# Kernel tuning notes

Hardware: AMD Instinct MI355X
Metric: run time of the kernel (lower is better)

The kernel has to match this reference:

```python
import math
import jax, jax.numpy as jnp
import numpy as np

N_HEAD = 16

def setup_inputs() -> dict:
    key = jax.random.key(0)
    k1, k2, k3 = jax.random.split(key, 3)
    B, T, C = 4, 2048, 1024
    x = jax.random.normal(k1, (B, T, C), dtype=jnp.float32)
    Wqkv = jax.random.normal(k2, (C, 3 * C), dtype=jnp.float32) * (1.0 / math.sqrt(C))
    bqkv = jnp.zeros((3 * C,), dtype=jnp.float32)
    Wproj = jax.random.normal(k3, (C, C), dtype=jnp.float32) * (1.0 / math.sqrt(C))
    bproj = jnp.zeros((C,), dtype=jnp.float32)
    return {"x": x, "Wqkv": Wqkv, "bqkv": bqkv, "Wproj": Wproj, "bproj": bproj}

def reference(x, Wqkv, bqkv, Wproj, bproj):
    B, T, C = x.shape
    H = N_HEAD
    D = C // H
    # fused QKV projection
    qkv = x @ Wqkv + bqkv                      # [B,T,3C]
    qkv = qkv.reshape(B, T, 3, H, D).transpose(0, 2, 3, 1, 4)  # [B,3,H,T,D]
    q, k, v = qkv[:, 0], qkv[:, 1], qkv[:, 2]  # each [B,H,T,D]
    scale = 1.0 / math.sqrt(D)
    att = jnp.einsum('bhtd,bhsd->bhts', q, k) * scale  # [B,H,T,T]
    # causal mask: disallow s > t
    mask = jnp.triu(jnp.ones((T, T), dtype=bool), k=1)
    att = jnp.where(mask, jnp.float32(-1e9), att)
    att = jax.nn.softmax(att, axis=-1)
    y = jnp.einsum('bhts,bhsd->bhtd', att, v)  # [B,H,T,D]
    y = y.transpose(0, 2, 1, 3).reshape(B, T, C)
    y = y @ Wproj + bproj
    return y
```

## Files before the change

### kernel.cpp

```cpp
#include <hip/hip_runtime.h>
#include <hip/hip_bf16.h>

#define B_ 4
#define T_ 2048
#define C_ 1024
#define H_ 16
#define D_ 64

typedef __attribute__((ext_vector_type(8))) short short8;
typedef __attribute__((ext_vector_type(4))) float f32x4;

#define QSCALE 0.18033688011112042f

static __device__ __forceinline__ unsigned short f2bf(float f) {
  unsigned u = __float_as_uint(f);
  u += 0x7fff + ((u >> 16) & 1);
  return (unsigned short)(u >> 16);
}

static __device__ __forceinline__ unsigned cvt_pk_bf16(float lo, float hi) {
  unsigned r;
  asm("v_cvt_pk_bf16_f32 %0, %1, %2" : "=v"(r) : "v"(lo), "v"(hi));
  return r;
}

static __device__ __forceinline__ float fast_exp2(float x) {
#if __has_builtin(__builtin_amdgcn_exp2f)
  return __builtin_amdgcn_exp2f(x);
#else
  return exp2f(x);
#endif
}

#define GL2LDS16(g, l)                                              \
  __builtin_amdgcn_global_load_lds(                                 \
      (const __attribute__((address_space(1))) void*)(g),           \
      (__attribute__((address_space(3))) void*)(l), 16, 0, 0)

__global__ __launch_bounds__(256) void prepass(
    const float* __restrict__ x, const float* __restrict__ Wq,
    const float* __restrict__ Wp, ushort* __restrict__ xb,
    ushort* __restrict__ Wqt, ushort* __restrict__ Wpt) {
  __shared__ ushort tile[32][33];
  const int bid = blockIdx.x;
  if (bid < 8192) {
    const size_t i = ((size_t)bid * 256 + threadIdx.x) * 4;
    float4 vv = *(const float4*)(x + i);
    ushort4 o = {f2bf(vv.x), f2bf(vv.y), f2bf(vv.z), f2bf(vv.w)};
    *(ushort4*)(xb + i) = o;
    return;
  }
  const float* in;
  ushort* out;
  int N, tix;
  if (bid < 8192 + 3072) {
    in = Wq; out = Wqt; N = 3 * C_; tix = bid - 8192;
  } else {
    in = Wp; out = Wpt; N = C_; tix = bid - 11264;
  }
  const int nT = N >> 5;
  const int k0 = (tix / nT) << 5, n0 = (tix % nT) << 5;
  const int r = threadIdx.x >> 3;
  const int c4 = (threadIdx.x & 7) << 2;
  float4 v = *(const float4*)(in + (size_t)(k0 + r) * N + n0 + c4);
  tile[c4 + 0][r] = f2bf(v.x);
  tile[c4 + 1][r] = f2bf(v.y);
  tile[c4 + 2][r] = f2bf(v.z);
  tile[c4 + 3][r] = f2bf(v.w);
  __syncthreads();
  ushort4 o = {tile[r][c4], tile[r][c4 + 1], tile[r][c4 + 2], tile[r][c4 + 3]};
  *(ushort4*)(out + (size_t)(n0 + r) * C_ + k0 + c4) = o;
}

static __device__ __forceinline__ void swz_src64(int wave, int lane, int p,
                                                 int& row, int& offU) {
  const int flat = p * 4096 + wave * 1024 + lane * 16;
  row = flat >> 7;
  const int pos = (flat & 127) >> 4;
  const int x = pos ^ (row & 7);
  offU = x * 8;
}
static __device__ __forceinline__ int swz_frag64(int r, int quad, int ko) {
  return r * 128 + (((quad | (ko << 2)) ^ (r & 7)) << 4);
}

__global__ __launch_bounds__(512, 2) void gemm_qkv_mfma(
    const ushort* __restrict__ A, const ushort* __restrict__ Bt,
    const float* __restrict__ bias, ushort* __restrict__ q,
    ushort* __restrict__ k, ushort* __restrict__ v) {
  __shared__ __align__(16) ushort KA[3][128 * 64];
  __shared__ __align__(16) ushort KB[3][256 * 64];
  const int wave = threadIdx.x >> 6, lane = threadIdx.x & 63;
  const int c = lane & 15, quad = lane >> 4;
  const int wm = wave >> 2, wn = wave & 3;
  const int bid0 = blockIdx.x;
  const int bid = (bid0 & 7) * 96 + (bid0 >> 3);
  const int m0 = (bid / 12) << 7;
  const int n0 = (bid % 12) << 8;

  int aRow[2], aX[2], bRow[4], bX[4];
#pragma unroll
  for (int p = 0; p < 2; ++p) {
    const int flat = p * 8192 + (int)threadIdx.x * 16;
    aRow[p] = flat >> 7;
    aX[p] = (((flat & 127) >> 4) ^ (aRow[p] & 7)) * 8;
  }
#pragma unroll
  for (int p = 0; p < 4; ++p) {
    const int flat = p * 8192 + (int)threadIdx.x * 16;
    bRow[p] = flat >> 7;
    bX[p] = (((flat & 127) >> 4) ^ (bRow[p] & 7)) * 8;
  }
  int fOffA[2][4], fOffB[2][4];
#pragma unroll
  for (int ko = 0; ko < 2; ++ko) {
#pragma unroll
    for (int i = 0; i < 4; ++i)
      fOffA[ko][i] = swz_frag64(wm * 64 + i * 16 + c, quad, ko);
#pragma unroll
    for (int j = 0; j < 4; ++j)
      fOffB[ko][j] = swz_frag64(wn * 64 + j * 16 + c, quad, ko);
  }

  f32x4 acc[4][4];
#pragma unroll
  for (int i = 0; i < 4; ++i)
#pragma unroll
    for (int j = 0; j < 4; ++j) acc[i][j] = (f32x4){0.f, 0.f, 0.f, 0.f};

#pragma unroll
  for (int p = 0; p < 4; ++p)
    GL2LDS16(Bt + (size_t)(n0 + bRow[p]) * C_ + bX[p],
             (char*)KB[0] + p * 8192 + wave * 1024);
#pragma unroll
  for (int p = 0; p < 2; ++p)
    GL2LDS16(A + (size_t)(m0 + aRow[p]) * C_ + aX[p],
             (char*)KA[0] + p * 8192 + wave * 1024);
#pragma unroll
  for (int p = 0; p < 4; ++p)
    GL2LDS16(Bt + (size_t)(n0 + bRow[p]) * C_ + 64 + bX[p],
             (char*)KB[1] + p * 8192 + wave * 1024);
#pragma unroll
  for (int p = 0; p < 2; ++p)
    GL2LDS16(A + (size_t)(m0 + aRow[p]) * C_ + 64 + aX[p],
             (char*)KA[1] + p * 8192 + wave * 1024);
  asm volatile("s_waitcnt vmcnt(6)" ::: "memory");
  __builtin_amdgcn_s_barrier();

  short8 af[4][2], bfA[2][2], bfB[2][2];
  {
    const char* la0 = (const char*)KA[0];
    const char* lb0 = (const char*)KB[0];
#pragma unroll
    for (int i = 0; i < 4; ++i)
#pragma unroll
      for (int ko = 0; ko < 2; ++ko)
        af[i][ko] = *(const short8*)(la0 + fOffA[ko][i]);
#pragma unroll
    for (int d = 0; d < 2; ++d)
#pragma unroll
      for (int ko = 0; ko < 2; ++ko)
        bfA[d][ko] = *(const short8*)(lb0 + fOffB[ko][d]);
  }

  int cur = 0;
  for (int kt = 0; kt < 16; ++kt) {
    const int nxt = (cur == 2) ? 0 : cur + 1;
    const int s2 = (nxt == 2) ? 0 : nxt + 1;
    const char* lb = (const char*)KB[cur];
    const int kk2 = (kt + 2) << 6;
    const bool more = (kt + 2) < 16;

#pragma unroll
    for (int d = 0; d < 2; ++d)
#pragma unroll
      for (int ko = 0; ko < 2; ++ko)
        bfB[d][ko] = *(const short8*)(lb + fOffB[ko][2 + d]);
    if (more) {
      GL2LDS16(Bt + (size_t)(n0 + bRow[0]) * C_ + kk2 + bX[0],
               (char*)KB[s2] + 0 * 8192 + wave * 1024);
      GL2LDS16(Bt + (size_t)(n0 + bRow[1]) * C_ + kk2 + bX[1],
               (char*)KB[s2] + 1 * 8192 + wave * 1024);
      GL2LDS16(A + (size_t)(m0 + aRow[0]) * C_ + kk2 + aX[0],
               (char*)KA[s2] + 0 * 8192 + wave * 1024);
    }
    __builtin_amdgcn_s_setprio(1);
#pragma unroll
    for (int i = 0; i < 4; ++i)
#pragma unroll
      for (int dj = 0; dj < 2; ++dj)
#pragma unroll
        for (int ko = 0; ko < 2; ++ko)
          acc[i][dj] = __builtin_amdgcn_mfma_f32_16x16x32_bf16(
              af[i][ko], bfA[dj][ko], acc[i][dj], 0, 0, 0);
    __builtin_amdgcn_s_setprio(0);

    if (more)
      asm volatile("s_waitcnt vmcnt(3) lgkmcnt(0)" ::: "memory");
    else
      asm volatile("s_waitcnt vmcnt(0) lgkmcnt(0)" ::: "memory");
    __builtin_amdgcn_s_barrier();

    short8 afN[4][2], bfAN[2][2];
    if (kt + 1 < 16) {
      const char* lan = (const char*)KA[nxt];
      const char* lbn = (const char*)KB[nxt];
#pragma unroll
      for (int i = 0; i < 4; ++i)
#pragma unroll
        for (int ko = 0; ko < 2; ++ko)
          afN[i][ko] = *(const short8*)(lan + fOffA[ko][i]);
#pragma unroll
      for (int d = 0; d < 2; ++d)
#pragma unroll
        for (int ko = 0; ko < 2; ++ko)
          bfAN[d][ko] = *(const short8*)(lbn + fOffB[ko][d]);
    }
    if (more) {
      GL2LDS16(Bt + (size_t)(n0 + bRow[2]) * C_ + kk2 + bX[2],
               (char*)KB[s2] + 2 * 8192 + wave * 1024);
      GL2LDS16(Bt + (size_t)(n0 + bRow[3]) * C_ + kk2 + bX[3],
               (char*)KB[s2] + 3 * 8192 + wave * 1024);
      GL2LDS16(A + (size_t)(m0 + aRow[1]) * C_ + kk2 + aX[1],
               (char*)KA[s2] + 1 * 8192 + wave * 1024);
    }
    __builtin_amdgcn_s_setprio(1);
#pragma unroll
    for (int i = 0; i < 4; ++i)
#pragma unroll
      for (int dj = 0; dj < 2; ++dj)
#pragma unroll
        for (int ko = 0; ko < 2; ++ko)
          acc[i][2 + dj] = __builtin_amdgcn_mfma_f32_16x16x32_bf16(
              af[i][ko], bfB[dj][ko], acc[i][2 + dj], 0, 0, 0);
    __builtin_amdgcn_s_setprio(0);
    if (kt + 1 < 16) {
#pragma unroll
      for (int i = 0; i < 4; ++i)
#pragma unroll
        for (int ko = 0; ko < 2; ++ko) af[i][ko] = afN[i][ko];
#pragma unroll
      for (int d = 0; d < 2; ++d)
#pragma unroll
        for (int ko = 0; ko < 2; ++ko) bfA[d][ko] = bfAN[d][ko];
    }
    cur = nxt;
  }

  const int s = n0 >> 10;
  if (s == 2) {
#pragma unroll
    for (int j = 0; j < 4; ++j) {
      const int n = n0 + wn * 64 + j * 16 + c;
      const int h = (n >> 6) & 15, d = n & 63;
      const float bval = bias[n];
#pragma unroll
      for (int i = 0; i < 4; ++i) {
        const int m = m0 + wm * 64 + i * 16 + quad * 4;
        const int b = m >> 11, t = m & 2047;
        ushort4 pk = {f2bf(acc[i][j][0] + bval), f2bf(acc[i][j][1] + bval),
                      f2bf(acc[i][j][2] + bval), f2bf(acc[i][j][3] + bval)};
        *(ushort4*)(v + (((size_t)((b << 4) + h) << 6) + d) * T_ + t) = pk;
      }
    }
  } else {
    ushort* outp = (s == 0) ? q : k;
    const float sc = (s == 0) ? QSCALE : 1.0f;
#pragma unroll
    for (int j = 0; j < 4; ++j) {
      const int n = n0 + wn * 64 + j * 16 + c;
      const int h = (n >> 6) & 15, d = n & 63;
      const float bval = bias[n];
#pragma unroll
      for (int i = 0; i < 4; ++i) {
#pragma unroll
        for (int r = 0; r < 4; ++r) {
          const int m = m0 + wm * 64 + i * 16 + quad * 4 + r;
          const int b = m >> 11, t = m & 2047;
          outp[(((size_t)((b << 4) + h) << 11) + t) * 64 + d] =
              f2bf((acc[i][j][r] + bval) * sc);
        }
      }
    }
  }
}

__global__ __launch_bounds__(256) void gemm_proj_mfma(
    const ushort* __restrict__ A, const ushort* __restrict__ Bt,
    const float* __restrict__ bias, float* __restrict__ out) {
  __shared__ __align__(16) ushort As[2][128 * 64];
  __shared__ __align__(16) ushort Bs[2][128 * 64];
  const int tid = threadIdx.x;
  const int wave = tid >> 6, lane = tid & 63;
  const int c = lane & 15, quad = lane >> 4;
  const int wm = wave & 1, wn = wave >> 1;
  const int bid0 = blockIdx.y * 8 + blockIdx.x;
  const int bid = (bid0 & 7) * 64 + (bid0 >> 3);
  const int m0 = (bid >> 3) << 7;
  const int n0 = (bid & 7) << 7;

  int sRow[4], sOff[4];
#pragma unroll
  for (int p = 0; p < 4; ++p) swz_src64(wave, lane, p, sRow[p], sOff[p]);
  int fOffA[2][4], fOffB[2][4];
#pragma unroll
  for (int ko = 0; ko < 2; ++ko) {
#pragma unroll
    for (int i = 0; i < 4; ++i)
      fOffA[ko][i] = swz_frag64(wm * 64 + i * 16 + c, quad, ko);
#pragma unroll
    for (int j = 0; j < 4; ++j)
      fOffB[ko][j] = swz_frag64(wn * 64 + j * 16 + c, quad, ko);
  }

  f32x4 acc[4][4];
#pragma unroll
  for (int i = 0; i < 4; ++i)
#pragma unroll
    for (int j = 0; j < 4; ++j) acc[i][j] = (f32x4){0.f, 0.f, 0.f, 0.f};

#define PROJ_STAGE(buf, kk)                                            \
  do {                                                                 \
    _Pragma("unroll") for (int p = 0; p < 4; ++p) {                    \
      GL2LDS16(A + (size_t)(m0 + sRow[p]) * C_ + (kk) + sOff[p],       \
               (char*)As[buf] + p * 4096 + wave * 1024);               \
      GL2LDS16(Bt + (size_t)(n0 + sRow[p]) * C_ + (kk) + sOff[p],      \
               (char*)Bs[buf] + p * 4096 + wave * 1024);               \
    }                                                                  \
  } while (0)

  PROJ_STAGE(0, 0);
  int cur = 0;
  for (int k0 = 0; k0 < C_; k0 += 64) {
    __syncthreads();
    if (k0 + 64 < C_) PROJ_STAGE(cur ^ 1, k0 + 64);
#pragma unroll
    for (int ko = 0; ko < 2; ++ko) {
      short8 af[4], bf[4];
#pragma unroll
      for (int i = 0; i < 4; ++i)
        af[i] = *(const short8*)((const char*)As[cur] + fOffA[ko][i]);
#pragma unroll
      for (int j = 0; j < 4; ++j)
        bf[j] = *(const short8*)((const char*)Bs[cur] + fOffB[ko][j]);
      __builtin_amdgcn_s_setprio(1);
#pragma unroll
      for (int i = 0; i < 4; ++i)
#pragma unroll
        for (int j = 0; j < 4; ++j)
          acc[i][j] = __builtin_amdgcn_mfma_f32_16x16x32_bf16(af[i], bf[j],
                                                              acc[i][j], 0, 0, 0);
      __builtin_amdgcn_s_setprio(0);
    }
    cur ^= 1;
  }
#undef PROJ_STAGE

#pragma unroll
  for (int j = 0; j < 4; ++j) {
    const int n = n0 + wn * 64 + j * 16 + c;
    const float bval = bias[n];
#pragma unroll
    for (int i = 0; i < 4; ++i) {
#pragma unroll
      for (int r = 0; r < 4; ++r) {
        const int m = m0 + wm * 64 + i * 16 + quad * 4 + r;
        out[(size_t)m * C_ + n] = acc[i][j][r] + bval;
      }
    }
  }
}

__global__ __launch_bounds__(256) void attn(const ushort* __restrict__ q,
                                            const ushort* __restrict__ k,
                                            const ushort* __restrict__ v,
                                            ushort* __restrict__ y2) {
  const int qt = 15 - (int)(blockIdx.x >> 6);
  const int bh = blockIdx.x & 63;
  const int t0 = qt << 7;
  const int w = threadIdx.x >> 6;
  const int lane = threadIdx.x & 63;
  const int c = lane & 15;
  const int quad = lane >> 4;

  const ushort* qp = q + (size_t)bh * T_ * D_;
  const ushort* kp = k + (size_t)bh * T_ * D_;
  const ushort* vp = v + (size_t)bh * D_ * T_;

  __shared__ __align__(16) ushort Ks[2][64 * 64];
  __shared__ __align__(16) ushort Vs[2][64 * 64];
  __shared__ __align__(16) ushort Ps[4][32][72];

  short8 qf[2][2];
#pragma unroll
  for (int g = 0; g < 2; ++g) {
    const ushort* qrow = qp + (size_t)(t0 + 32 * w + 16 * g + c) * D_;
    qf[g][0] = *(const short8*)(qrow + quad * 8);
    qf[g][1] = *(const short8*)(qrow + 32 + quad * 8);
  }

  int sRow[2], sX[2];
#pragma unroll
  for (int p = 0; p < 2; ++p) {
    const int flat = p * 4096 + (int)threadIdx.x * 16;
    sRow[p] = flat >> 7;
    sX[p] = (((flat & 127) >> 4) ^ (sRow[p] & 7)) * 8;
  }

#define STAGE(buf, s0s)                                                   \
  do {                                                                    \
    _Pragma("unroll") for (int p = 0; p < 2; ++p) {                       \
      GL2LDS16(kp + (size_t)((s0s) + sRow[p]) * D_ + sX[p],               \
               (char*)Ks[buf] + p * 4096 + w * 1024);                     \
      GL2LDS16(vp + (size_t)sRow[p] * T_ + (s0s) + sX[p],                 \
               (char*)Vs[buf] + p * 4096 + w * 1024);                     \
    }                                                                     \
  } while (0)

  f32x4 o[2][4];
  float l_i[2] = {0.f, 0.f};
#pragma unroll
  for (int g = 0; g < 2; ++g)
#pragma unroll
    for (int dt = 0; dt < 4; ++dt) o[g][dt] = (f32x4){0.f, 0.f, 0.f, 0.f};

  const int nb = 2 * qt + 2;
  STAGE(0, 0);
  int cur = 0;

  for (int ib = 0; ib < nb; ++ib) {
    const int s0 = ib << 6;
    __syncthreads();
    if (ib + 1 < nb) STAGE(cur ^ 1, s0 + 64);

    f32x4 st[2][4];
    __builtin_amdgcn_s_setprio(1);
#pragma unroll
    for (int kt = 0; kt < 4; ++kt) {
      const char* kb = (const char*)Ks[cur];
      short8 af0 = *(const short8*)(kb + swz_frag64(kt * 16 + c, quad, 0));
      short8 af1 = *(const short8*)(kb + swz_frag64(kt * 16 + c, quad, 1));
#pragma unroll
      for (int g = 0; g < 2; ++g) {
        f32x4 a = (f32x4){0.f, 0.f, 0.f, 0.f};
        a = __builtin_amdgcn_mfma_f32_16x16x32_bf16(af0, qf[g][0], a, 0, 0, 0);
        a = __builtin_amdgcn_mfma_f32_16x16x32_bf16(af1, qf[g][1], a, 0, 0, 0);
        st[g][kt] = a;
      }
    }
    __builtin_amdgcn_s_setprio(0);

#pragma unroll
    for (int g = 0; g < 2; ++g) {
      const int qbase = t0 + 32 * w + 16 * g;
      if (s0 + 63 > qbase) {
#pragma unroll
        for (int kt = 0; kt < 4; ++kt)
#pragma unroll
          for (int r = 0; r < 4; ++r)
            if (s0 + kt * 16 + 4 * quad + r > qbase + c) st[g][kt][r] = -1e30f;
      }
      float lacc = 0.f;
#pragma unroll
      for (int kt = 0; kt < 4; ++kt) {
        float p0 = fast_exp2(st[g][kt][0]);
        float p1 = fast_exp2(st[g][kt][1]);
        float p2 = fast_exp2(st[g][kt][2]);
        float p3 = fast_exp2(st[g][kt][3]);
        lacc += (p0 + p1) + (p2 + p3);
        uint2 pw = {cvt_pk_bf16(p0, p1), cvt_pk_bf16(p2, p3)};
        *(uint2*)(&Ps[w][g * 16 + c][kt * 16 + 4 * quad]) = pw;
      }
      l_i[g] += lacc;
    }

    short8 pf[2][2];
#pragma unroll
    for (int g = 0; g < 2; ++g) {
      pf[g][0] = *(const short8*)(&Ps[w][g * 16 + c][quad * 8]);
      pf[g][1] = *(const short8*)(&Ps[w][g * 16 + c][32 + quad * 8]);
    }
    __builtin_amdgcn_s_setprio(1);
#pragma unroll
    for (int dt = 0; dt < 4; ++dt) {
      const char* vb = (const char*)Vs[cur];
      short8 vf0 = *(const short8*)(vb + swz_frag64(dt * 16 + c, quad, 0));
      short8 vf1 = *(const short8*)(vb + swz_frag64(dt * 16 + c, quad, 1));
#pragma unroll
      for (int g = 0; g < 2; ++g) {
        o[g][dt] =
            __builtin_amdgcn_mfma_f32_16x16x32_bf16(vf0, pf[g][0], o[g][dt], 0, 0, 0);
        o[g][dt] =
            __builtin_amdgcn_mfma_f32_16x16x32_bf16(vf1, pf[g][1], o[g][dt], 0, 0, 0);
      }
    }
    __builtin_amdgcn_s_setprio(0);
    cur ^= 1;
  }
#undef STAGE

  float linv[2];
#pragma unroll
  for (int g = 0; g < 2; ++g) {
    float ls = l_i[g];
    ls += __shfl_xor(ls, 16);
    ls += __shfl_xor(ls, 32);
    linv[g] = 1.0f / ls;
  }

  const int b = bh >> 4, h = bh & 15;
#pragma unroll
  for (int g = 0; g < 2; ++g) {
    const int row = t0 + 32 * w + 16 * g + c;
    ushort* dst = y2 + (size_t)(b * T_ + row) * C_ + h * 64;
#pragma unroll
    for (int dt = 0; dt < 4; ++dt) {
      uint2 ov = {cvt_pk_bf16(o[g][dt][0] * linv[g], o[g][dt][1] * linv[g]),
                  cvt_pk_bf16(o[g][dt][2] * linv[g], o[g][dt][3] * linv[g])};
      *(uint2*)(dst + dt * 16 + 4 * quad) = ov;
    }
  }
}

extern "C" void kernel_launch(void* const* d_in, const int* in_sizes, int n_in,
                              void* d_out, int out_size, void* d_ws,
                              size_t ws_size, hipStream_t stream) {
  const float* x = (const float*)d_in[0];
  const float* Wqkv = (const float*)d_in[1];
  const float* bqkv = (const float*)d_in[2];
  const float* Wproj = (const float*)d_in[3];
  const float* bproj = (const float*)d_in[4];
  float* out = (float*)d_out;

  const size_t per = (size_t)B_ * H_ * T_ * D_;
  ushort* q = (ushort*)d_ws;
  ushort* k = q + per;
  ushort* v = k + per;
  ushort* y2 = v + per;
  ushort* xb = y2 + per;
  ushort* Wqkvt = xb + per;
  ushort* Wprojt = Wqkvt + 3 * C_ * C_;

  prepass<<<dim3(12288), 256, 0, stream>>>(x, Wqkv, Wproj, xb, Wqkvt, Wprojt);
  gemm_qkv_mfma<<<dim3(768), 512, 0, stream>>>(xb, Wqkvt, bqkv, q, k, v);
  attn<<<dim3(1024), 256, 0, stream>>>(q, k, v, y2);
  gemm_proj_mfma<<<dim3(8, 64), 256, 0, stream>>>(y2, Wprojt, bproj, out);
}
```

Measured before the change: 238.2 us.

## Use persistent attention blocks with atomic work queue and XCD-aware QKV tile mapping

```diff
diff --git a/kernel.cpp b/kernel.cpp
--- a/kernel.cpp
+++ b/kernel.cpp
@@ -40,9 +40,11 @@
 __global__ __launch_bounds__(256) void prepass(
     const float* __restrict__ x, const float* __restrict__ Wq,
     const float* __restrict__ Wp, ushort* __restrict__ xb,
-    ushort* __restrict__ Wqt, ushort* __restrict__ Wpt) {
+    ushort* __restrict__ Wqt, ushort* __restrict__ Wpt,
+    unsigned* __restrict__ ctr) {
   __shared__ ushort tile[32][33];
   const int bid = blockIdx.x;
+  if (bid == 0 && threadIdx.x == 0) *ctr = 0u;
   if (bid < 8192) {
     const size_t i = ((size_t)bid * 256 + threadIdx.x) * 4;
     float4 vv = *(const float4*)(x + i);
@@ -94,9 +96,9 @@
   const int c = lane & 15, quad = lane >> 4;
   const int wm = wave >> 2, wn = wave & 3;
   const int bid0 = blockIdx.x;
-  const int bid = (bid0 & 7) * 96 + (bid0 >> 3);
-  const int m0 = (bid / 12) << 7;
-  const int n0 = (bid % 12) << 8;
+  const int xcd = bid0 & 7, r0 = bid0 >> 3;
+  const int m0 = (((xcd >> 1) << 4) + r0 / 6) << 7;
+  const int n0 = ((xcd & 1) * 6 + r0 % 6) << 8;
 
   int aRow[2], aX[2], bRow[4], bX[4];
 #pragma unroll
@@ -374,30 +376,17 @@
 __global__ __launch_bounds__(256) void attn(const ushort* __restrict__ q,
                                             const ushort* __restrict__ k,
                                             const ushort* __restrict__ v,
-                                            ushort* __restrict__ y2) {
-  const int qt = 15 - (int)(blockIdx.x >> 6);
-  const int bh = blockIdx.x & 63;
-  const int t0 = qt << 7;
+                                            ushort* __restrict__ y2,
+                                            unsigned* __restrict__ ctr) {
   const int w = threadIdx.x >> 6;
   const int lane = threadIdx.x & 63;
   const int c = lane & 15;
   const int quad = lane >> 4;
 
-  const ushort* qp = q + (size_t)bh * T_ * D_;
-  const ushort* kp = k + (size_t)bh * T_ * D_;
-  const ushort* vp = v + (size_t)bh * D_ * T_;
-
   __shared__ __align__(16) ushort Ks[2][64 * 64];
   __shared__ __align__(16) ushort Vs[2][64 * 64];
   __shared__ __align__(16) ushort Ps[4][32][72];
-
-  short8 qf[2][2];
-#pragma unroll
-  for (int g = 0; g < 2; ++g) {
-    const ushort* qrow = qp + (size_t)(t0 + 32 * w + 16 * g + c) * D_;
-    qf[g][0] = *(const short8*)(qrow + quad * 8);
-    qf[g][1] = *(const short8*)(qrow + 32 + quad * 8);
-  }
+  __shared__ unsigned item_s;
 
   int sRow[2], sX[2];
 #pragma unroll
@@ -406,6 +395,29 @@
     sRow[p] = flat >> 7;
     sX[p] = (((flat & 127) >> 4) ^ (sRow[p] & 7)) * 8;
   }
+
+  for (;;) {
+    if (threadIdx.x == 0) item_s = atomicAdd(ctr, 1u);
+    __syncthreads();
+    const unsigned item = item_s;
+    __syncthreads();
+    if (item >= 1024u) return;
+
+    const int qt = 15 - (int)(item >> 6);
+    const int bh = (int)(item & 63u);
+    const int t0 = qt << 7;
+
+    const ushort* qp = q + (size_t)bh * T_ * D_;
+    const ushort* kp = k + (size_t)bh * T_ * D_;
+    const ushort* vp = v + (size_t)bh * D_ * T_;
+
+    short8 qf[2][2];
+#pragma unroll
+    for (int g = 0; g < 2; ++g) {
+      const ushort* qrow = qp + (size_t)(t0 + 32 * w + 16 * g + c) * D_;
+      qf[g][0] = *(const short8*)(qrow + quad * 8);
+      qf[g][1] = *(const short8*)(qrow + 32 + quad * 8);
+    }
 
 #define STAGE(buf, s0s)                                                   \
   do {                                                                    \
@@ -417,107 +429,108 @@
     }                                                                     \
   } while (0)
 
-  f32x4 o[2][4];
-  float l_i[2] = {0.f, 0.f};
-#pragma unroll
-  for (int g = 0; g < 2; ++g)
-#pragma unroll
-    for (int dt = 0; dt < 4; ++dt) o[g][dt] = (f32x4){0.f, 0.f, 0.f, 0.f};
-
-  const int nb = 2 * qt + 2;
-  STAGE(0, 0);
-  int cur = 0;
-
-  for (int ib = 0; ib < nb; ++ib) {
-    const int s0 = ib << 6;
-    __syncthreads();
-    if (ib + 1 < nb) STAGE(cur ^ 1, s0 + 64);
-
-    f32x4 st[2][4];
-    __builtin_amdgcn_s_setprio(1);
-#pragma unroll
-    for (int kt = 0; kt < 4; ++kt) {
-      const char* kb = (const char*)Ks[cur];
-      short8 af0 = *(const short8*)(kb + swz_frag64(kt * 16 + c, quad, 0));
-      short8 af1 = *(const short8*)(kb + swz_frag64(kt * 16 + c, quad, 1));
+    f32x4 o[2][4];
+    float l_i[2] = {0.f, 0.f};
+#pragma unroll
+    for (int g = 0; g < 2; ++g)
+#pragma unroll
+      for (int dt = 0; dt < 4; ++dt) o[g][dt] = (f32x4){0.f, 0.f, 0.f, 0.f};
+
+    const int nb = 2 * qt + 2;
+    STAGE(0, 0);
+    int cur = 0;
+
+    for (int ib = 0; ib < nb; ++ib) {
+      const int s0 = ib << 6;
+      __syncthreads();
+      if (ib + 1 < nb) STAGE(cur ^ 1, s0 + 64);
+
+      f32x4 st[2][4];
+      __builtin_amdgcn_s_setprio(1);
+#pragma unroll
+      for (int kt = 0; kt < 4; ++kt) {
+        const char* kb = (const char*)Ks[cur];
+        short8 af0 = *(const short8*)(kb + swz_frag64(kt * 16 + c, quad, 0));
+        short8 af1 = *(const short8*)(kb + swz_frag64(kt * 16 + c, quad, 1));
+#pragma unroll
+        for (int g = 0; g < 2; ++g) {
+          f32x4 a = (f32x4){0.f, 0.f, 0.f, 0.f};
+          a = __builtin_amdgcn_mfma_f32_16x16x32_bf16(af0, qf[g][0], a, 0, 0, 0);
+          a = __builtin_amdgcn_mfma_f32_16x16x32_bf16(af1, qf[g][1], a, 0, 0, 0);
+          st[g][kt] = a;
+        }
+      }
+      __builtin_amdgcn_s_setprio(0);
+
 #pragma unroll
       for (int g = 0; g < 2; ++g) {
-        f32x4 a = (f32x4){0.f, 0.f, 0.f, 0.f};
-        a = __builtin_amdgcn_mfma_f32_16x16x32_bf16(af0, qf[g][0], a, 0, 0, 0);
-        a = __builtin_amdgcn_mfma_f32_16x16x32_bf16(af1, qf[g][1], a, 0, 0, 0);
-        st[g][kt] = a;
-      }
-    }
-    __builtin_amdgcn_s_setprio(0);
-
+        const int qbase = t0 + 32 * w + 16 * g;
+        if (s0 + 63 > qbase) {
+#pragma unroll
+          for (int kt = 0; kt < 4; ++kt)
+#pragma unroll
+            for (int r = 0; r < 4; ++r)
+              if (s0 + kt * 16 + 4 * quad + r > qbase + c) st[g][kt][r] = -1e30f;
+        }
+        float lacc = 0.f;
+#pragma unroll
+        for (int kt = 0; kt < 4; ++kt) {
+          float p0 = fast_exp2(st[g][kt][0]);
+          float p1 = fast_exp2(st[g][kt][1]);
+          float p2 = fast_exp2(st[g][kt][2]);
+          float p3 = fast_exp2(st[g][kt][3]);
+          lacc += (p0 + p1) + (p2 + p3);
+          uint2 pw = {cvt_pk_bf16(p0, p1), cvt_pk_bf16(p2, p3)};
+          *(uint2*)(&Ps[w][g * 16 + c][kt * 16 + 4 * quad]) = pw;
+        }
+        l_i[g] += lacc;
+      }
+
+      short8 pf[2][2];
+#pragma unroll
+      for (int g = 0; g < 2; ++g) {
+        pf[g][0] = *(const short8*)(&Ps[w][g * 16 + c][quad * 8]);
+        pf[g][1] = *(const short8*)(&Ps[w][g * 16 + c][32 + quad * 8]);
+      }
+      __builtin_amdgcn_s_setprio(1);
+#pragma unroll
+      for (int dt = 0; dt < 4; ++dt) {
+        const char* vb = (const char*)Vs[cur];
+        short8 vf0 = *(const short8*)(vb + swz_frag64(dt * 16 + c, quad, 0));
+        short8 vf1 = *(const short8*)(vb + swz_frag64(dt * 16 + c, quad, 1));
+#pragma unroll
+        for (int g = 0; g < 2; ++g) {
+          o[g][dt] = __builtin_amdgcn_mfma_f32_16x16x32_bf16(vf0, pf[g][0],
+                                                             o[g][dt], 0, 0, 0);
+          o[g][dt] = __builtin_amdgcn_mfma_f32_16x16x32_bf16(vf1, pf[g][1],
+                                                             o[g][dt], 0, 0, 0);
+        }
+      }
+      __builtin_amdgcn_s_setprio(0);
+      cur ^= 1;
+    }
+#undef STAGE
+
+    float linv[2];
 #pragma unroll
     for (int g = 0; g < 2; ++g) {
-      const int qbase = t0 + 32 * w + 16 * g;
-      if (s0 + 63 > qbase) {
-#pragma unroll
-        for (int kt = 0; kt < 4; ++kt)
-#pragma unroll
-          for (int r = 0; r < 4; ++r)
-            if (s0 + kt * 16 + 4 * quad + r > qbase + c) st[g][kt][r] = -1e30f;
-      }
-      float lacc = 0.f;
-#pragma unroll
-      for (int kt = 0; kt < 4; ++kt) {
-        float p0 = fast_exp2(st[g][kt][0]);
-        float p1 = fast_exp2(st[g][kt][1]);
-        float p2 = fast_exp2(st[g][kt][2]);
-        float p3 = fast_exp2(st[g][kt][3]);
-        lacc += (p0 + p1) + (p2 + p3);
-        uint2 pw = {cvt_pk_bf16(p0, p1), cvt_pk_bf16(p2, p3)};
-        *(uint2*)(&Ps[w][g * 16 + c][kt * 16 + 4 * quad]) = pw;
-      }
-      l_i[g] += lacc;
-    }
-
-    short8 pf[2][2];
+      float ls = l_i[g];
+      ls += __shfl_xor(ls, 16);
+      ls += __shfl_xor(ls, 32);
+      linv[g] = 1.0f / ls;
+    }
+
+    const int b = bh >> 4, h = bh & 15;
 #pragma unroll
     for (int g = 0; g < 2; ++g) {
-      pf[g][0] = *(const short8*)(&Ps[w][g * 16 + c][quad * 8]);
-      pf[g][1] = *(const short8*)(&Ps[w][g * 16 + c][32 + quad * 8]);
-    }
-    __builtin_amdgcn_s_setprio(1);
-#pragma unroll
-    for (int dt = 0; dt < 4; ++dt) {
-      const char* vb = (const char*)Vs[cur];
-      short8 vf0 = *(const short8*)(vb + swz_frag64(dt * 16 + c, quad, 0));
-      short8 vf1 = *(const short8*)(vb + swz_frag64(dt * 16 + c, quad, 1));
-#pragma unroll
-      for (int g = 0; g < 2; ++g) {
-        o[g][dt] =
-            __builtin_amdgcn_mfma_f32_16x16x32_bf16(vf0, pf[g][0], o[g][dt], 0, 0, 0);
-        o[g][dt] =
-            __builtin_amdgcn_mfma_f32_16x16x32_bf16(vf1, pf[g][1], o[g][dt], 0, 0, 0);
-      }
-    }
-    __builtin_amdgcn_s_setprio(0);
-    cur ^= 1;
-  }
-#undef STAGE
-
-  float linv[2];
-#pragma unroll
-  for (int g = 0; g < 2; ++g) {
-    float ls = l_i[g];
-    ls += __shfl_xor(ls, 16);
-    ls += __shfl_xor(ls, 32);
-    linv[g] = 1.0f / ls;
-  }
-
-  const int b = bh >> 4, h = bh & 15;
-#pragma unroll
-  for (int g = 0; g < 2; ++g) {
-    const int row = t0 + 32 * w + 16 * g + c;
-    ushort* dst = y2 + (size_t)(b * T_ + row) * C_ + h * 64;
-#pragma unroll
-    for (int dt = 0; dt < 4; ++dt) {
-      uint2 ov = {cvt_pk_bf16(o[g][dt][0] * linv[g], o[g][dt][1] * linv[g]),
-                  cvt_pk_bf16(o[g][dt][2] * linv[g], o[g][dt][3] * linv[g])};
-      *(uint2*)(dst + dt * 16 + 4 * quad) = ov;
+      const int row = t0 + 32 * w + 16 * g + c;
+      ushort* dst = y2 + (size_t)(b * T_ + row) * C_ + h * 64;
+#pragma unroll
+      for (int dt = 0; dt < 4; ++dt) {
+        uint2 ov = {cvt_pk_bf16(o[g][dt][0] * linv[g], o[g][dt][1] * linv[g]),
+                    cvt_pk_bf16(o[g][dt][2] * linv[g], o[g][dt][3] * linv[g])};
+        *(uint2*)(dst + dt * 16 + 4 * quad) = ov;
+      }
     }
   }
 }
@@ -540,9 +553,11 @@
   ushort* xb = y2 + per;
   ushort* Wqkvt = xb + per;
   ushort* Wprojt = Wqkvt + 3 * C_ * C_;
-
-  prepass<<<dim3(12288), 256, 0, stream>>>(x, Wqkv, Wproj, xb, Wqkvt, Wprojt);
+  unsigned* ctr = (unsigned*)(Wprojt + (size_t)C_ * C_);
+
+  prepass<<<dim3(12288), 256, 0, stream>>>(x, Wqkv, Wproj, xb, Wqkvt, Wprojt,
+                                           ctr);
   gemm_qkv_mfma<<<dim3(768), 512, 0, stream>>>(xb, Wqkvt, bqkv, q, k, v);
-  attn<<<dim3(1024), 256, 0, stream>>>(q, k, v, y2);
+  attn<<<dim3(768), 256, 0, stream>>>(q, k, v, y2, ctr);
   gemm_proj_mfma<<<dim3(8, 64), 256, 0, stream>>>(y2, Wprojt, bproj, out);
 }
```

Result: slower. 248.2 us (+4.2%).
